# Performance work log

Measured on AMD Instinct MI355X. Metric: run time of the kernel, lower is better.

The kernel has to match this reference:

```python
import jax, jax.numpy as jnp
import numpy as np

D_MODEL = 1024
N_HEADS = 16
HEAD_DIM = D_MODEL // N_HEADS
SEQ_LEN = 2048
BATCH = 4


def setup_inputs() -> dict:
    key = jax.random.key(0)
    k1, k2, k3 = jax.random.split(key, 3)
    x = jax.random.normal(k1, (BATCH, SEQ_LEN, D_MODEL), dtype=jnp.float32)
    # Linear weights stored as [in, out] so y = x @ W (equivalent to torch x @ W.T)
    w_qkv = jax.random.normal(k2, (D_MODEL, 3 * D_MODEL), dtype=jnp.float32) * (D_MODEL ** -0.5)
    w_proj = jax.random.normal(k3, (D_MODEL, D_MODEL), dtype=jnp.float32) * (D_MODEL ** -0.5)
    return {"x": x, "w_qkv": w_qkv, "w_proj": w_proj}


def reference(x, w_qkv, w_proj):
    B, T, C = x.shape
    qkv = x @ w_qkv  # [B, T, 3C]
    q, k, v = jnp.split(qkv, 3, axis=-1)
    # [B, H, T, hd]
    q = q.reshape(B, T, N_HEADS, HEAD_DIM).transpose(0, 2, 1, 3)
    k = k.reshape(B, T, N_HEADS, HEAD_DIM).transpose(0, 2, 1, 3)
    v = v.reshape(B, T, N_HEADS, HEAD_DIM).transpose(0, 2, 1, 3)
    scale = HEAD_DIM ** -0.5
    attn = jnp.einsum("bhqd,bhkd->bhqk", q, k) * scale  # [B, H, T, T]
    causal = jnp.tril(jnp.ones((T, T), dtype=bool))
    attn = jnp.where(causal, attn, -jnp.inf)
    attn = jax.nn.softmax(attn, axis=-1)
    out = jnp.einsum("bhqk,bhkd->bhqd", attn, v)  # [B, H, T, hd]
    out = out.transpose(0, 2, 1, 3).reshape(B, T, C)
    return out @ w_proj
```

## Files before the change

kernel.cpp:

```cpp
#include <hip/hip_runtime.h>
#include <stdint.h>


typedef __bf16 bf16x8 __attribute__((ext_vector_type(8)));
typedef float f32x4 __attribute__((ext_vector_type(4)));
typedef unsigned short u16x8 __attribute__((ext_vector_type(8)));

#define DEVINL static __device__ __forceinline__

DEVINL unsigned short f2b(float f) {
  __bf16 h = (__bf16)f;
  return __builtin_bit_cast(unsigned short, h);
}

DEVINL void gld16(const void* g, void* l) {
  __builtin_amdgcn_global_load_lds(
      (const __attribute__((address_space(1))) void*)g,
      (__attribute__((address_space(3))) void*)l, 16, 0, 0);
}

DEVINL f32x4 mfma16(bf16x8 a, bf16x8 b, f32x4 c) {
  return __builtin_amdgcn_mfma_f32_16x16x32_bf16(a, b, c, 0, 0, 0);
}

#define SCHED_FENCE() __builtin_amdgcn_sched_barrier(0)

__global__ __launch_bounds__(256) void k_cast_bf16(const float* __restrict__ in,
                                                   unsigned short* __restrict__ out,
                                                   int n8) {
  int i = blockIdx.x * 256 + threadIdx.x;
  if (i >= n8) return;
  const float4* p = (const float4*)in + (size_t)i * 2;
  float4 a = p[0], b = p[1];
  u16x8 o;
  o[0] = f2b(a.x); o[1] = f2b(a.y); o[2] = f2b(a.z); o[3] = f2b(a.w);
  o[4] = f2b(b.x); o[5] = f2b(b.y); o[6] = f2b(b.z); o[7] = f2b(b.w);
  *(u16x8*)(out + (size_t)i * 8) = o;
}

__global__ __launch_bounds__(256) void k_transpose_w(const float* __restrict__ in,
                                                     unsigned short* __restrict__ out,
                                                     int R, int C) {
  __shared__ float t[64][65];
  int ci = blockIdx.x * 64, ri = blockIdx.y * 64;
  int tid = threadIdx.x;
#pragma unroll
  for (int j = 0; j < 4; ++j) {
    int c = tid + j * 256;
    int row = c >> 4;
    int col = (c & 15) * 4;
    float4 v = *(const float4*)(in + (size_t)(ri + row) * C + ci + col);
    t[row][col] = v.x; t[row][col + 1] = v.y; t[row][col + 2] = v.z; t[row][col + 3] = v.w;
  }
  __syncthreads();
  int cc = tid >> 2;
  int seg = (tid & 3) * 16;
  u16x8 o0, o1;
#pragma unroll
  for (int j = 0; j < 8; ++j) o0[j] = f2b(t[seg + j][cc]);
#pragma unroll
  for (int j = 0; j < 8; ++j) o1[j] = f2b(t[seg + 8 + j][cc]);
  unsigned short* dst = out + (size_t)(ci + cc) * R + ri + seg;
  *(u16x8*)dst = o0;
  *(u16x8*)(dst + 8) = o1;
}

__global__ __launch_bounds__(256) void k_transpose_v(const unsigned short* __restrict__ v,
                                                     unsigned short* __restrict__ vt) {
  __shared__ unsigned short s[64][65];
  int bh = blockIdx.y;
  int t0 = blockIdx.x * 64;
  int tid = threadIdx.x;
  const unsigned short* src = v + ((size_t)bh * 2048 + t0) * 64;
#pragma unroll
  for (int j = 0; j < 2; ++j) {
    int c = tid + j * 256;
    int row = c >> 3;
    int col = (c & 7) * 8;
    u16x8 x = *(const u16x8*)(src + (size_t)row * 64 + col);
#pragma unroll
    for (int q = 0; q < 8; ++q) s[row][col + q] = x[q];
  }
  __syncthreads();
  int d = tid >> 2;
  int seg = (tid & 3) * 16;
  u16x8 o0, o1;
#pragma unroll
  for (int j = 0; j < 8; ++j) o0[j] = s[seg + j][d];
#pragma unroll
  for (int j = 0; j < 8; ++j) o1[j] = s[seg + 8 + j][d];
  unsigned short* dst = vt + ((size_t)bh * 64 + d) * 2048 + t0 + seg;
  *(u16x8*)dst = o0;
  *(u16x8*)(dst + 8) = o1;
}

template <int MODE>
__global__ __launch_bounds__(256) void k_gemm(const unsigned short* __restrict__ A,
                                              const unsigned short* __restrict__ Bt,
                                              int M, int N, int K,
                                              float* __restrict__ Cf,
                                              unsigned short* __restrict__ qo,
                                              unsigned short* __restrict__ ko,
                                              unsigned short* __restrict__ vo,
                                              float qscale) {
  __shared__ unsigned short As[2][128 * 32];
  __shared__ unsigned short Bs[2][128 * 32];
  int tid = threadIdx.x;
  int w = tid >> 6, lane = tid & 63, l15 = lane & 15, l4 = lane >> 4;
  int nwg = gridDim.x;
  int gy = M >> 7;
  int lin = blockIdx.x;
  int nx = nwg >> 3, rr = nwg & 7;
  int xcd = lin & 7, idx = lin >> 3;
  int wgid = (xcd < rr ? xcd * (nx + 1) : rr * (nx + 1) + (xcd - rr) * nx) + idx;
  int bn = wgid / gy, bm = wgid % gy;
  int wr = (w >> 1) * 64, wc = (w & 1) * 64;
  f32x4 acc[4][4];
#pragma unroll
  for (int i = 0; i < 4; ++i)
#pragma unroll
    for (int j = 0; j < 4; ++j) acc[i][j] = (f32x4){0.f, 0.f, 0.f, 0.f};
  const char* Ab = (const char*)(A + (size_t)bm * 128 * K);
  const char* Bb = (const char*)(Bt + (size_t)bn * 128 * K);
  int c_0 = tid, c_1 = tid + 256;
  int row0 = c_0 >> 2, cb0 = (c_0 & 3) * 16;
  int row1 = c_1 >> 2, cb1 = (c_1 & 3) * 16;

  auto stage = [&](int kt, int buf) {
    gld16(Ab + ((size_t)row0 * K + kt) * 2 + cb0, (char*)As[buf] + c_0 * 16);
    gld16(Bb + ((size_t)row0 * K + kt) * 2 + cb0, (char*)Bs[buf] + c_0 * 16);
    gld16(Ab + ((size_t)row1 * K + kt) * 2 + cb1, (char*)As[buf] + c_1 * 16);
    gld16(Bb + ((size_t)row1 * K + kt) * 2 + cb1, (char*)Bs[buf] + c_1 * 16);
  };

  const int nkt = K >> 5;
  stage(0, 0);
  SCHED_FENCE();
  for (int t = 0; t < nkt; ++t) {
    int cur = t & 1;
    if (t) {
      SCHED_FENCE();
      __builtin_amdgcn_s_barrier();
      SCHED_FENCE();
    }
    if (t + 1 < nkt) {
      stage((t + 1) * 32, cur ^ 1);
      SCHED_FENCE();
      asm volatile("s_waitcnt vmcnt(4)" ::: "memory");
    } else {
      SCHED_FENCE();
      asm volatile("s_waitcnt vmcnt(0)" ::: "memory");
    }
    SCHED_FENCE();
    __builtin_amdgcn_s_barrier();
    SCHED_FENCE();
    const char* Ac = (const char*)As[cur];
    const char* Bc = (const char*)Bs[cur];
    bf16x8 af[4], bfr[4];
#pragma unroll
    for (int m = 0; m < 4; ++m)
      af[m] = *(const bf16x8*)(Ac + (wr + m * 16 + l15) * 64 + l4 * 16);
#pragma unroll
    for (int n = 0; n < 4; ++n)
      bfr[n] = *(const bf16x8*)(Bc + (wc + n * 16 + l15) * 64 + l4 * 16);
    __builtin_amdgcn_s_setprio(1);
#pragma unroll
    for (int m = 0; m < 4; ++m)
#pragma unroll
      for (int n = 0; n < 4; ++n)
        acc[m][n] = mfma16(af[m], bfr[n], acc[m][n]);
    __builtin_amdgcn_s_setprio(0);
  }
#pragma unroll
  for (int m = 0; m < 4; ++m) {
    int grow0 = bm * 128 + wr + m * 16 + l4 * 4;
#pragma unroll
    for (int n = 0; n < 4; ++n) {
      int gcol = bn * 128 + wc + n * 16 + l15;
#pragma unroll
      for (int r = 0; r < 4; ++r) {
        int grow = grow0 + r;
        float val = acc[m][n][r];
        if (MODE == 1) {
          Cf[(size_t)grow * N + gcol] = val;
        } else {
          int which = gcol >> 10, rem = gcol & 1023;
          int h = rem >> 6, d = rem & 63;
          int b = grow >> 11, t = grow & 2047;
          size_t off = (((size_t)(b * 16 + h)) * 2048 + t) * 64 + d;
          if (which == 0)      qo[off] = f2b(val * qscale);
          else if (which == 1) ko[off] = f2b(val);
          else                 vo[off] = f2b(val);
        }
      }
    }
  }
}

__global__ __launch_bounds__(256) void k_attn(const unsigned short* __restrict__ Q,
                                              const unsigned short* __restrict__ Kt,
                                              const unsigned short* __restrict__ Vt,
                                              unsigned short* __restrict__ AO) {
  __shared__ unsigned short Ks[2][4096];
  __shared__ unsigned short Vs[2][4096];
  __shared__ unsigned short Ps[4096];
  int tid = threadIdx.x;
  int w = tid >> 6, lane = tid & 63, l15 = lane & 15, l4 = lane >> 4;
  int lin = blockIdx.x;
  int xcd = lin & 7, jj = lin >> 3;
  int bh = xcd * 8 + (jj & 7);
  int p = jj >> 3;
  const char* Kb = (const char*)(Kt + (size_t)bh * 2048 * 64);
  const char* Vb = (const char*)(Vt + (size_t)bh * 64 * 2048);
  const int swp = (l15 & 7) << 4;
  char* Pw = (char*)Ps + w * 2048;
  int b = bh >> 4, h = bh & 15;

  int Lb0 = (w * 64 + lane) * 16;
  int Lb1 = ((w + 4) * 64 + lane) * 16;
  int Nb0 = Lb0 ^ (((Lb0 >> 7) & 7) << 4);
  int Nb1 = Lb1 ^ (((Lb1 >> 7) & 7) << 4);
  int d0 = Nb0 >> 7, in0 = Nb0 & 127;
  int d1 = Nb1 >> 7, in1 = Nb1 & 127;

  auto stage = [&](int t, int buf) {
    size_t kv0 = (size_t)t * 64;
    gld16(Kb + kv0 * 128 + Nb0, (char*)Ks[buf] + Lb0);
    gld16(Vb + (size_t)d0 * 4096 + kv0 * 2 + in0, (char*)Vs[buf] + Lb0);
    gld16(Kb + kv0 * 128 + Nb1, (char*)Ks[buf] + Lb1);
    gld16(Vb + (size_t)d1 * 4096 + kv0 * 2 + in1, (char*)Vs[buf] + Lb1);
  };

  auto run = [&](int qi) {
    int q0 = qi * 64;
    const unsigned short* Qb = Q + ((size_t)bh * 2048 + q0 + w * 16) * 64;
    bf16x8 qf0 = *(const bf16x8*)((const char*)Qb + l15 * 128 + l4 * 16);
    bf16x8 qf1 = *(const bf16x8*)((const char*)Qb + l15 * 128 + 64 + l4 * 16);
    f32x4 o[4];
#pragma unroll
    for (int i = 0; i < 4; ++i) o[i] = (f32x4){0.f, 0.f, 0.f, 0.f};
    float mrow = -1e30f, lrow = 0.f;
    const int ntiles = qi + 1;
    const int qg = w * 16 + l15;
    SCHED_FENCE();
    __builtin_amdgcn_s_barrier();
    SCHED_FENCE();
    stage(0, 0);
    SCHED_FENCE();
    for (int it = 0; it < ntiles; ++it) {
      int cur = it & 1;
      if (it) {
        SCHED_FENCE();
        __builtin_amdgcn_s_barrier();
        SCHED_FENCE();
      }
      if (it + 1 < ntiles) {
        stage(it + 1, cur ^ 1);
        SCHED_FENCE();
        asm volatile("s_waitcnt vmcnt(4)" ::: "memory");
      } else {
        SCHED_FENCE();
        asm volatile("s_waitcnt vmcnt(0)" ::: "memory");
      }
      SCHED_FENCE();
      __builtin_amdgcn_s_barrier();
      SCHED_FENCE();
      const char* Kc = (const char*)Ks[cur];
      const char* Vc = (const char*)Vs[cur];
      f32x4 s[4];
      __builtin_amdgcn_s_setprio(1);
#pragma unroll
      for (int c = 0; c < 4; ++c) {
        int row = c * 16 + l15;
        int base = row * 128 + l4 * 16;
        int sw = (row & 7) << 4;
        bf16x8 k0 = *(const bf16x8*)(Kc + (base ^ sw));
        bf16x8 k1 = *(const bf16x8*)(Kc + ((base + 64) ^ sw));
        f32x4 t = mfma16(k0, qf0, (f32x4){0.f, 0.f, 0.f, 0.f});
        s[c] = mfma16(k1, qf1, t);
      }
      __builtin_amdgcn_s_setprio(0);
      if (it == ntiles - 1) {
#pragma unroll
        for (int c = 0; c < 4; ++c) {
          int kvb = c * 16 + l4 * 4;
#pragma unroll
          for (int r = 0; r < 4; ++r)
            if (kvb + r > qg) s[c][r] = -1e30f;
        }
      }
      float mx = fmaxf(fmaxf(fmaxf(s[0][0], s[0][1]), fmaxf(s[0][2], s[0][3])),
                       fmaxf(fmaxf(s[1][0], s[1][1]), fmaxf(s[1][2], s[1][3])));
      mx = fmaxf(mx, fmaxf(fmaxf(fmaxf(s[2][0], s[2][1]), fmaxf(s[2][2], s[2][3])),
                           fmaxf(fmaxf(s[3][0], s[3][1]), fmaxf(s[3][2], s[3][3]))));
      mx = fmaxf(mx, __shfl_xor(mx, 16));
      mx = fmaxf(mx, __shfl_xor(mx, 32));
      float mn = fmaxf(mrow, mx);
      float corr = __builtin_amdgcn_exp2f(mrow - mn);
      mrow = mn;
      float rs = 0.f;
#pragma unroll
      for (int c = 0; c < 4; ++c) {
        float p0 = __builtin_amdgcn_exp2f(s[c][0] - mn);
        float p1 = __builtin_amdgcn_exp2f(s[c][1] - mn);
        float p2 = __builtin_amdgcn_exp2f(s[c][2] - mn);
        float p3 = __builtin_amdgcn_exp2f(s[c][3] - mn);
        rs += (p0 + p1) + (p2 + p3);
        uint32_t lo = (uint32_t)f2b(p0) | ((uint32_t)f2b(p1) << 16);
        uint32_t hi = (uint32_t)f2b(p2) | ((uint32_t)f2b(p3) << 16);
        *(uint2*)(Pw + ((l15 * 128 + c * 32 + l4 * 8) ^ swp)) = make_uint2(lo, hi);
      }
      rs += __shfl_xor(rs, 16);
      rs += __shfl_xor(rs, 32);
      lrow = lrow * corr + rs;
      float corr_r[4];
#pragma unroll
      for (int r = 0; r < 4; ++r) corr_r[r] = __shfl(corr, l4 * 4 + r);
#pragma unroll
      for (int dc = 0; dc < 4; ++dc)
#pragma unroll
        for (int r = 0; r < 4; ++r) o[dc][r] *= corr_r[r];
      bf16x8 pa[2];
#pragma unroll
      for (int kc = 0; kc < 2; ++kc)
        pa[kc] = *(const bf16x8*)(Pw + ((l15 * 128 + kc * 64 + l4 * 16) ^ swp));
      __builtin_amdgcn_s_setprio(1);
#pragma unroll
      for (int dc = 0; dc < 4; ++dc) {
#pragma unroll
        for (int kc = 0; kc < 2; ++kc) {
          int vrow = dc * 16 + l15;
          int vnat = vrow * 128 + kc * 64 + l4 * 16;
          bf16x8 vb = *(const bf16x8*)(Vc + (vnat ^ ((vrow & 7) << 4)));
          o[dc] = mfma16(pa[kc], vb, o[dc]);
        }
      }
      __builtin_amdgcn_s_setprio(0);
    }
    float inv[4];
#pragma unroll
    for (int r = 0; r < 4; ++r) inv[r] = 1.f / __shfl(lrow, l4 * 4 + r);
#pragma unroll
    for (int dc = 0; dc < 4; ++dc) {
#pragma unroll
      for (int r = 0; r < 4; ++r) {
        int t = q0 + w * 16 + l4 * 4 + r;
        AO[((size_t)(b * 2048 + t)) * 1024 + h * 64 + dc * 16 + l15] =
            f2b(o[dc][r] * inv[r]);
      }
    }
  };

  run(31 - p);
  run(p);
}

extern "C" void kernel_launch(void* const* d_in, const int* in_sizes, int n_in,
                              void* d_out, int out_size, void* d_ws, size_t ws_size,
                              hipStream_t stream) {
  const float* x      = (const float*)d_in[0];
  const float* w_qkv  = (const float*)d_in[1];
  const float* w_proj = (const float*)d_in[2];
  float* out = (float*)d_out;
  char* ws = (char*)d_ws;
  const size_t MB = 1024 * 1024;
  unsigned short* xb     = (unsigned short*)(ws);
  unsigned short* vT     = (unsigned short*)(ws);
  unsigned short* wqkvT  = (unsigned short*)(ws + 16 * MB);
  unsigned short* wprojT = (unsigned short*)(ws + 22 * MB);
  unsigned short* q      = (unsigned short*)(ws + 24 * MB);
  unsigned short* k      = (unsigned short*)(ws + 40 * MB);
  unsigned short* v      = (unsigned short*)(ws + 56 * MB);
  unsigned short* ao     = (unsigned short*)(ws + 56 * MB);

  k_cast_bf16<<<4096, 256, 0, stream>>>(x, xb, 1048576);
  k_transpose_w<<<dim3(48, 16), 256, 0, stream>>>(w_qkv, wqkvT, 1024, 3072);
  k_transpose_w<<<dim3(16, 16), 256, 0, stream>>>(w_proj, wprojT, 1024, 1024);
  const float qscale = 0.125f * 1.44269504088896f;
  k_gemm<0><<<1536, 256, 0, stream>>>(xb, wqkvT, 8192, 3072, 1024,
                                      nullptr, q, k, v, qscale);
  k_transpose_v<<<dim3(32, 64), 256, 0, stream>>>(v, vT);
  k_attn<<<1024, 256, 0, stream>>>(q, k, vT, ao);
  k_gemm<1><<<512, 256, 0, stream>>>(ao, wprojT, 8192, 1024, 1024,
                                     out, nullptr, nullptr, nullptr, 1.f);
}
```

Before: 202.4 us.

## Fuse V transpose into QKV GEMM epilogue and widen attention tiles to 128 queries

The QKV GEMM epilogue now writes V directly in transposed [bh, d, t] layout using packed 4-element stores, which removes the separate transpose kernel and its extra round trip through memory. The attention kernel moves to 512 threads (8 waves) per block handling 128 query rows, so each K/V tile staged in LDS is shared by twice as many waves. Each thread now issues one staging load per tile instead of two. Waves skip KV tiles that lie fully above their causal diagonal. This trades fewer blocks (512) and idle waves on diagonal tiles for more K/V reuse per load.

```diff
diff --git a/kernel.cpp b/kernel.cpp
--- a/kernel.cpp
+++ b/kernel.cpp
@@ -61,35 +61,6 @@
 #pragma unroll
   for (int j = 0; j < 8; ++j) o1[j] = f2b(t[seg + 8 + j][cc]);
   unsigned short* dst = out + (size_t)(ci + cc) * R + ri + seg;
-  *(u16x8*)dst = o0;
-  *(u16x8*)(dst + 8) = o1;
-}
-
-__global__ __launch_bounds__(256) void k_transpose_v(const unsigned short* __restrict__ v,
-                                                     unsigned short* __restrict__ vt) {
-  __shared__ unsigned short s[64][65];
-  int bh = blockIdx.y;
-  int t0 = blockIdx.x * 64;
-  int tid = threadIdx.x;
-  const unsigned short* src = v + ((size_t)bh * 2048 + t0) * 64;
-#pragma unroll
-  for (int j = 0; j < 2; ++j) {
-    int c = tid + j * 256;
-    int row = c >> 3;
-    int col = (c & 7) * 8;
-    u16x8 x = *(const u16x8*)(src + (size_t)row * 64 + col);
-#pragma unroll
-    for (int q = 0; q < 8; ++q) s[row][col + q] = x[q];
-  }
-  __syncthreads();
-  int d = tid >> 2;
-  int seg = (tid & 3) * 16;
-  u16x8 o0, o1;
-#pragma unroll
-  for (int j = 0; j < 8; ++j) o0[j] = s[seg + j][d];
-#pragma unroll
-  for (int j = 0; j < 8; ++j) o1[j] = s[seg + 8 + j][d];
-  unsigned short* dst = vt + ((size_t)bh * 64 + d) * 2048 + t0 + seg;
   *(u16x8*)dst = o0;
   *(u16x8*)(dst + 8) = o1;
 }
@@ -177,33 +148,40 @@
 #pragma unroll
     for (int n = 0; n < 4; ++n) {
       int gcol = bn * 128 + wc + n * 16 + l15;
-#pragma unroll
-      for (int r = 0; r < 4; ++r) {
-        int grow = grow0 + r;
-        float val = acc[m][n][r];
-        if (MODE == 1) {
-          Cf[(size_t)grow * N + gcol] = val;
+      if (MODE == 1) {
+#pragma unroll
+        for (int r = 0; r < 4; ++r)
+          Cf[(size_t)(grow0 + r) * N + gcol] = acc[m][n][r];
+      } else {
+        int which = gcol >> 10, rem = gcol & 1023;
+        int h = rem >> 6, d = rem & 63;
+        int b = grow0 >> 11, t0 = grow0 & 2047;
+        if (which == 2) {
+          uint32_t lo = (uint32_t)f2b(acc[m][n][0]) | ((uint32_t)f2b(acc[m][n][1]) << 16);
+          uint32_t hi = (uint32_t)f2b(acc[m][n][2]) | ((uint32_t)f2b(acc[m][n][3]) << 16);
+          size_t off = (((size_t)(b * 16 + h)) * 64 + d) * 2048 + t0;
+          *(uint2*)(vo + off) = make_uint2(lo, hi);
         } else {
-          int which = gcol >> 10, rem = gcol & 1023;
-          int h = rem >> 6, d = rem & 63;
-          int b = grow >> 11, t = grow & 2047;
-          size_t off = (((size_t)(b * 16 + h)) * 2048 + t) * 64 + d;
-          if (which == 0)      qo[off] = f2b(val * qscale);
-          else if (which == 1) ko[off] = f2b(val);
-          else                 vo[off] = f2b(val);
+          size_t off = (((size_t)(b * 16 + h)) * 2048 + t0) * 64 + d;
+#pragma unroll
+          for (int r = 0; r < 4; ++r) {
+            float val = acc[m][n][r];
+            if (which == 0) qo[off + (size_t)r * 64] = f2b(val * qscale);
+            else            ko[off + (size_t)r * 64] = f2b(val);
+          }
         }
       }
     }
   }
 }
 
-__global__ __launch_bounds__(256) void k_attn(const unsigned short* __restrict__ Q,
+__global__ __launch_bounds__(512) void k_attn(const unsigned short* __restrict__ Q,
                                               const unsigned short* __restrict__ Kt,
                                               const unsigned short* __restrict__ Vt,
                                               unsigned short* __restrict__ AO) {
   __shared__ unsigned short Ks[2][4096];
   __shared__ unsigned short Vs[2][4096];
-  __shared__ unsigned short Ps[4096];
+  __shared__ unsigned short Ps[8192];
   int tid = threadIdx.x;
   int w = tid >> 6, lane = tid & 63, l15 = lane & 15, l4 = lane >> 4;
   int lin = blockIdx.x;
@@ -216,23 +194,18 @@
   char* Pw = (char*)Ps + w * 2048;
   int b = bh >> 4, h = bh & 15;
 
-  int Lb0 = (w * 64 + lane) * 16;
-  int Lb1 = ((w + 4) * 64 + lane) * 16;
+  int Lb0 = tid * 16;
   int Nb0 = Lb0 ^ (((Lb0 >> 7) & 7) << 4);
-  int Nb1 = Lb1 ^ (((Lb1 >> 7) & 7) << 4);
   int d0 = Nb0 >> 7, in0 = Nb0 & 127;
-  int d1 = Nb1 >> 7, in1 = Nb1 & 127;
 
   auto stage = [&](int t, int buf) {
     size_t kv0 = (size_t)t * 64;
     gld16(Kb + kv0 * 128 + Nb0, (char*)Ks[buf] + Lb0);
     gld16(Vb + (size_t)d0 * 4096 + kv0 * 2 + in0, (char*)Vs[buf] + Lb0);
-    gld16(Kb + kv0 * 128 + Nb1, (char*)Ks[buf] + Lb1);
-    gld16(Vb + (size_t)d1 * 4096 + kv0 * 2 + in1, (char*)Vs[buf] + Lb1);
   };
 
   auto run = [&](int qi) {
-    int q0 = qi * 64;
+    int q0 = qi * 128;
     const unsigned short* Qb = Q + ((size_t)bh * 2048 + q0 + w * 16) * 64;
     bf16x8 qf0 = *(const bf16x8*)((const char*)Qb + l15 * 128 + l4 * 16);
     bf16x8 qf1 = *(const bf16x8*)((const char*)Qb + l15 * 128 + 64 + l4 * 16);
@@ -240,8 +213,9 @@
 #pragma unroll
     for (int i = 0; i < 4; ++i) o[i] = (f32x4){0.f, 0.f, 0.f, 0.f};
     float mrow = -1e30f, lrow = 0.f;
-    const int ntiles = qi + 1;
-    const int qg = w * 16 + l15;
+    const int ntiles = 2 * qi + 2;
+    const int qgmin = q0 + w * 16;
+    const int qg = qgmin + l15;
     SCHED_FENCE();
     __builtin_amdgcn_s_barrier();
     SCHED_FENCE();
@@ -257,7 +231,7 @@
       if (it + 1 < ntiles) {
         stage(it + 1, cur ^ 1);
         SCHED_FENCE();
-        asm volatile("s_waitcnt vmcnt(4)" ::: "memory");
+        asm volatile("s_waitcnt vmcnt(2)" ::: "memory");
       } else {
         SCHED_FENCE();
         asm volatile("s_waitcnt vmcnt(0)" ::: "memory");
@@ -265,77 +239,79 @@
       SCHED_FENCE();
       __builtin_amdgcn_s_barrier();
       SCHED_FENCE();
-      const char* Kc = (const char*)Ks[cur];
-      const char* Vc = (const char*)Vs[cur];
-      f32x4 s[4];
-      __builtin_amdgcn_s_setprio(1);
-#pragma unroll
-      for (int c = 0; c < 4; ++c) {
-        int row = c * 16 + l15;
-        int base = row * 128 + l4 * 16;
-        int sw = (row & 7) << 4;
-        bf16x8 k0 = *(const bf16x8*)(Kc + (base ^ sw));
-        bf16x8 k1 = *(const bf16x8*)(Kc + ((base + 64) ^ sw));
-        f32x4 t = mfma16(k0, qf0, (f32x4){0.f, 0.f, 0.f, 0.f});
-        s[c] = mfma16(k1, qf1, t);
-      }
-      __builtin_amdgcn_s_setprio(0);
-      if (it == ntiles - 1) {
+      if (it * 64 <= qgmin + 15) {
+        const char* Kc = (const char*)Ks[cur];
+        const char* Vc = (const char*)Vs[cur];
+        f32x4 s[4];
+        __builtin_amdgcn_s_setprio(1);
 #pragma unroll
         for (int c = 0; c < 4; ++c) {
-          int kvb = c * 16 + l4 * 4;
-#pragma unroll
-          for (int r = 0; r < 4; ++r)
-            if (kvb + r > qg) s[c][r] = -1e30f;
-        }
-      }
-      float mx = fmaxf(fmaxf(fmaxf(s[0][0], s[0][1]), fmaxf(s[0][2], s[0][3])),
-                       fmaxf(fmaxf(s[1][0], s[1][1]), fmaxf(s[1][2], s[1][3])));
-      mx = fmaxf(mx, fmaxf(fmaxf(fmaxf(s[2][0], s[2][1]), fmaxf(s[2][2], s[2][3])),
-                           fmaxf(fmaxf(s[3][0], s[3][1]), fmaxf(s[3][2], s[3][3]))));
-      mx = fmaxf(mx, __shfl_xor(mx, 16));
-      mx = fmaxf(mx, __shfl_xor(mx, 32));
-      float mn = fmaxf(mrow, mx);
-      float corr = __builtin_amdgcn_exp2f(mrow - mn);
-      mrow = mn;
-      float rs = 0.f;
-#pragma unroll
-      for (int c = 0; c < 4; ++c) {
-        float p0 = __builtin_amdgcn_exp2f(s[c][0] - mn);
-        float p1 = __builtin_amdgcn_exp2f(s[c][1] - mn);
-        float p2 = __builtin_amdgcn_exp2f(s[c][2] - mn);
-        float p3 = __builtin_amdgcn_exp2f(s[c][3] - mn);
-        rs += (p0 + p1) + (p2 + p3);
-        uint32_t lo = (uint32_t)f2b(p0) | ((uint32_t)f2b(p1) << 16);
-        uint32_t hi = (uint32_t)f2b(p2) | ((uint32_t)f2b(p3) << 16);
-        *(uint2*)(Pw + ((l15 * 128 + c * 32 + l4 * 8) ^ swp)) = make_uint2(lo, hi);
-      }
-      rs += __shfl_xor(rs, 16);
-      rs += __shfl_xor(rs, 32);
-      lrow = lrow * corr + rs;
-      float corr_r[4];
-#pragma unroll
-      for (int r = 0; r < 4; ++r) corr_r[r] = __shfl(corr, l4 * 4 + r);
-#pragma unroll
-      for (int dc = 0; dc < 4; ++dc)
-#pragma unroll
-        for (int r = 0; r < 4; ++r) o[dc][r] *= corr_r[r];
-      bf16x8 pa[2];
-#pragma unroll
-      for (int kc = 0; kc < 2; ++kc)
-        pa[kc] = *(const bf16x8*)(Pw + ((l15 * 128 + kc * 64 + l4 * 16) ^ swp));
-      __builtin_amdgcn_s_setprio(1);
-#pragma unroll
-      for (int dc = 0; dc < 4; ++dc) {
-#pragma unroll
-        for (int kc = 0; kc < 2; ++kc) {
-          int vrow = dc * 16 + l15;
-          int vnat = vrow * 128 + kc * 64 + l4 * 16;
-          bf16x8 vb = *(const bf16x8*)(Vc + (vnat ^ ((vrow & 7) << 4)));
-          o[dc] = mfma16(pa[kc], vb, o[dc]);
-        }
-      }
-      __builtin_amdgcn_s_setprio(0);
+          int row = c * 16 + l15;
+          int base = row * 128 + l4 * 16;
+          int sw = (row & 7) << 4;
+          bf16x8 k0 = *(const bf16x8*)(Kc + (base ^ sw));
+          bf16x8 k1 = *(const bf16x8*)(Kc + ((base + 64) ^ sw));
+          f32x4 t = mfma16(k0, qf0, (f32x4){0.f, 0.f, 0.f, 0.f});
+          s[c] = mfma16(k1, qf1, t);
+        }
+        __builtin_amdgcn_s_setprio(0);
+        if (it * 64 + 63 > qgmin) {
+#pragma unroll
+          for (int c = 0; c < 4; ++c) {
+            int kvb = it * 64 + c * 16 + l4 * 4;
+#pragma unroll
+            for (int r = 0; r < 4; ++r)
+              if (kvb + r > qg) s[c][r] = -1e30f;
+          }
+        }
+        float mx = fmaxf(fmaxf(fmaxf(s[0][0], s[0][1]), fmaxf(s[0][2], s[0][3])),
+                         fmaxf(fmaxf(s[1][0], s[1][1]), fmaxf(s[1][2], s[1][3])));
+        mx = fmaxf(mx, fmaxf(fmaxf(fmaxf(s[2][0], s[2][1]), fmaxf(s[2][2], s[2][3])),
+                             fmaxf(fmaxf(s[3][0], s[3][1]), fmaxf(s[3][2], s[3][3]))));
+        mx = fmaxf(mx, __shfl_xor(mx, 16));
+        mx = fmaxf(mx, __shfl_xor(mx, 32));
+        float mn = fmaxf(mrow, mx);
+        float corr = __builtin_amdgcn_exp2f(mrow - mn);
+        mrow = mn;
+        float rs = 0.f;
+#pragma unroll
+        for (int c = 0; c < 4; ++c) {
+          float p0 = __builtin_amdgcn_exp2f(s[c][0] - mn);
+          float p1 = __builtin_amdgcn_exp2f(s[c][1] - mn);
+          float p2 = __builtin_amdgcn_exp2f(s[c][2] - mn);
+          float p3 = __builtin_amdgcn_exp2f(s[c][3] - mn);
+          rs += (p0 + p1) + (p2 + p3);
+          uint32_t lo = (uint32_t)f2b(p0) | ((uint32_t)f2b(p1) << 16);
+          uint32_t hi = (uint32_t)f2b(p2) | ((uint32_t)f2b(p3) << 16);
+          *(uint2*)(Pw + ((l15 * 128 + c * 32 + l4 * 8) ^ swp)) = make_uint2(lo, hi);
+        }
+        rs += __shfl_xor(rs, 16);
+        rs += __shfl_xor(rs, 32);
+        lrow = lrow * corr + rs;
+        float corr_r[4];
+#pragma unroll
+        for (int r = 0; r < 4; ++r) corr_r[r] = __shfl(corr, l4 * 4 + r);
+#pragma unroll
+        for (int dc = 0; dc < 4; ++dc)
+#pragma unroll
+          for (int r = 0; r < 4; ++r) o[dc][r] *= corr_r[r];
+        bf16x8 pa[2];
+#pragma unroll
+        for (int kc = 0; kc < 2; ++kc)
+          pa[kc] = *(const bf16x8*)(Pw + ((l15 * 128 + kc * 64 + l4 * 16) ^ swp));
+        __builtin_amdgcn_s_setprio(1);
+#pragma unroll
+        for (int dc = 0; dc < 4; ++dc) {
+#pragma unroll
+          for (int kc = 0; kc < 2; ++kc) {
+            int vrow = dc * 16 + l15;
+            int vnat = vrow * 128 + kc * 64 + l4 * 16;
+            bf16x8 vb = *(const bf16x8*)(Vc + (vnat ^ ((vrow & 7) << 4)));
+            o[dc] = mfma16(pa[kc], vb, o[dc]);
+          }
+        }
+        __builtin_amdgcn_s_setprio(0);
+      }
     }
     float inv[4];
 #pragma unroll
@@ -351,7 +327,7 @@
     }
   };
 
-  run(31 - p);
+  run(15 - p);
   run(p);
 }
 
@@ -365,22 +341,20 @@
   char* ws = (char*)d_ws;
   const size_t MB = 1024 * 1024;
   unsigned short* xb     = (unsigned short*)(ws);
-  unsigned short* vT     = (unsigned short*)(ws);
+  unsigned short* ao     = (unsigned short*)(ws);
   unsigned short* wqkvT  = (unsigned short*)(ws + 16 * MB);
   unsigned short* wprojT = (unsigned short*)(ws + 22 * MB);
   unsigned short* q      = (unsigned short*)(ws + 24 * MB);
   unsigned short* k      = (unsigned short*)(ws + 40 * MB);
-  unsigned short* v      = (unsigned short*)(ws + 56 * MB);
-  unsigned short* ao     = (unsigned short*)(ws + 56 * MB);
+  unsigned short* vT     = (unsigned short*)(ws + 56 * MB);
 
   k_cast_bf16<<<4096, 256, 0, stream>>>(x, xb, 1048576);
   k_transpose_w<<<dim3(48, 16), 256, 0, stream>>>(w_qkv, wqkvT, 1024, 3072);
   k_transpose_w<<<dim3(16, 16), 256, 0, stream>>>(w_proj, wprojT, 1024, 1024);
   const float qscale = 0.125f * 1.44269504088896f;
   k_gemm<0><<<1536, 256, 0, stream>>>(xb, wqkvT, 8192, 3072, 1024,
-                                      nullptr, q, k, v, qscale);
-  k_transpose_v<<<dim3(32, 64), 256, 0, stream>>>(v, vT);
-  k_attn<<<1024, 256, 0, stream>>>(q, k, vT, ao);
+                                      nullptr, q, k, vT, qscale);
+  k_attn<<<512, 512, 0, stream>>>(q, k, vT, ao);
   k_gemm<1><<<512, 256, 0, stream>>>(ao, wprojT, 8192, 1024, 1024,
                                      out, nullptr, nullptr, nullptr, 1.f);
 }
```

After: 190.7 us. 1.06x faster.
